# Kernel tuning notes

Measured on AMD Instinct MI355X. Metric: run time of the kernel, lower is better.

## Reference

```python
import jax, jax.numpy as jnp
import numpy as np

B, O, T, D, H, DOUT = 32, 4096, 16384, 128, 128, 128
EPS = 1e-3  # keras BatchNormalization default epsilon


def setup_inputs() -> dict:
    key = jax.random.key(0)
    ks = jax.random.split(key, 8)
    std = 0.05  # keras RandomNormal default stddev
    return {
        "obj_vecs": jax.random.normal(ks[0], (B, O, D), jnp.float32),
        "pred_vecs": jax.random.normal(ks[1], (B, T, D), jnp.float32),
        "edges": jax.random.randint(ks[2], (B, T, 2), 0, O, dtype=jnp.int32),
        # net1: [3D -> H] -> BN -> ReLU -> [H -> 2H+Dout] -> BN -> ReLU
        "W1": jax.random.normal(ks[3], (3 * D, H), jnp.float32) * std,
        "b1": jnp.zeros((H,), jnp.float32),
        "g1": jnp.ones((H,), jnp.float32),
        "be1": jnp.zeros((H,), jnp.float32),
        "W2": jax.random.normal(ks[4], (H, 2 * H + DOUT), jnp.float32) * std,
        "b2": jnp.zeros((2 * H + DOUT,), jnp.float32),
        "g2": jnp.ones((2 * H + DOUT,), jnp.float32),
        "be2": jnp.zeros((2 * H + DOUT,), jnp.float32),
        # net2: [H -> H] -> BN -> ReLU -> [H -> Dout] -> BN -> ReLU
        "W3": jax.random.normal(ks[5], (H, H), jnp.float32) * std,
        "b3": jnp.zeros((H,), jnp.float32),
        "g3": jnp.ones((H,), jnp.float32),
        "be3": jnp.zeros((H,), jnp.float32),
        "W4": jax.random.normal(ks[6], (H, DOUT), jnp.float32) * std,
        "b4": jnp.zeros((DOUT,), jnp.float32),
        "g4": jnp.ones((DOUT,), jnp.float32),
        "be4": jnp.zeros((DOUT,), jnp.float32),
    }


def _block(x, W, b, g, be):
    # Dense -> BatchNorm(inference: mean=0, var=1) -> ReLU
    h = x @ W + b
    h = h * (g / jnp.sqrt(1.0 + EPS)) + be
    return jax.nn.relu(h)


def reference(obj_vecs, pred_vecs, edges,
              W1, b1, g1, be1, W2, b2, g2, be2,
              W3, b3, g3, be3, W4, b4, g4, be4):
    s_idx = edges[..., 0]  # (B, T)
    o_idx = edges[..., 1]  # (B, T)

    # gather subject / object vectors: (B, T, D)
    cur_s = jnp.take_along_axis(obj_vecs, s_idx[..., None], axis=1)
    cur_o = jnp.take_along_axis(obj_vecs, o_idx[..., None], axis=1)
    cur_t = jnp.concatenate([cur_s, pred_vecs, cur_o], axis=2)  # (B, T, 3D)

    new_t = _block(_block(cur_t, W1, b1, g1, be1), W2, b2, g2, be2)  # (B, T, 2H+Dout)
    new_s = new_t[..., :H]
    new_p = new_t[..., H:H + DOUT]
    new_o = new_t[..., H + DOUT:]

    # NOTE: original TF code overwrites the s-scatter with the o-scatter,
    # so only object-side messages contribute. scatter_nd sums duplicates.
    bidx = jnp.arange(B)[:, None]  # (B, 1), broadcasts over T
    pooled = jnp.zeros((B, O, H), new_t.dtype).at[bidx, o_idx].add(new_o)
    counts = jnp.zeros((B, O), new_t.dtype).at[bidx, o_idx].add(1.0)
    pooled = pooled / jnp.clip(counts, 1.0, None)[..., None]  # avg pooling

    new_obj = _block(_block(pooled, W3, b3, g3, be3), W4, b4, g4, be4)  # (B, O, Dout)
    return new_obj, new_p
```

## Files before the change

### kernel.cpp

```cpp
#include <hip/hip_runtime.h>
#include <hip/hip_bf16.h>
#include <stdint.h>

#define Bn 32
#define On 4096
#define Tn 16384
#define Dn 128

typedef short short8 __attribute__((ext_vector_type(8)));
typedef float f32x4 __attribute__((ext_vector_type(4)));

__device__ inline short f2bf(float f) {
  union { float f; uint32_t u; } v; v.f = f;
  uint32_t u = v.u;
  uint32_t r = u + 0x7fffu + ((u >> 16) & 1u);
  return (short)(r >> 16);
}
__device__ inline float bf2f(unsigned short u) {
  union { uint32_t ui; float f; } cv; cv.ui = ((uint32_t)u) << 16; return cv.f;
}

#define LBAR() do { \
  asm volatile("s_waitcnt lgkmcnt(0)" ::: "memory"); \
  __builtin_amdgcn_sched_barrier(0); \
  __builtin_amdgcn_s_barrier(); \
} while (0)

__global__ void prep_weights(const float* __restrict__ W1, const float* __restrict__ W2,
                             const float* __restrict__ W3, const float* __restrict__ W4,
                             short* __restrict__ w1t, short* __restrict__ w2t,
                             short* __restrict__ w3t, short* __restrict__ w4t) {
  int i = blockIdx.x * 256 + threadIdx.x;
  if (i < 49152) {
    int n = i / 384, k = i % 384;
    w1t[i] = f2bf(W1[k * 128 + n]);
  } else if (i < 49152 + 32768) {
    int j = i - 49152;
    int n = j / 128, k = j % 128;
    w2t[j] = f2bf(W2[k * 384 + 128 + n]);
  } else if (i < 49152 + 32768 + 16384) {
    int j = i - 81920;
    int n = j / 128, k = j % 128;
    w3t[j] = f2bf(W3[k * 128 + n]);
  } else if (i < 114688) {
    int j = i - 98304;
    int n = j / 128, k = j % 128;
    w4t[j] = f2bf(W4[k * 128 + n]);
  }
}

__global__ __launch_bounds__(1024) void sort_kernel(
    const int* __restrict__ edges, int* __restrict__ hist_g,
    int* __restrict__ offs_g, unsigned short* __restrict__ eidx)
{
  __shared__ int h[4096];
  __shared__ int of[4096];
  __shared__ int sd[1024];
  int b = blockIdx.x, tid = threadIdx.x;
#pragma unroll
  for (int i = 0; i < 4; i++) h[tid + i * 1024] = 0;
  __syncthreads();
  int ov[16];
#pragma unroll
  for (int j = 0; j < 16; j++) {
    int t = j * 1024 + tid;
    ov[j] = edges[((size_t)(b * Tn + t)) * 2 + 1];
    atomicAdd(&h[ov[j]], 1);
  }
  __syncthreads();
  int base = tid * 4;
  int hh[4]; int s = 0;
#pragma unroll
  for (int j = 0; j < 4; j++) { hh[j] = h[base + j]; s += hh[j]; }
  sd[tid] = s;
  int tsum = s;
  for (int off = 1; off < 1024; off <<= 1) {
    __syncthreads();
    int t = (tid >= off) ? sd[tid - off] : 0;
    __syncthreads();
    sd[tid] += t;
  }
  __syncthreads();
  int excl = sd[tid] - tsum + b * Tn;
#pragma unroll
  for (int j = 0; j < 4; j++) {
    of[base + j] = excl;
    offs_g[b * On + base + j] = excl;
    hist_g[b * On + base + j] = hh[j];
    excl += hh[j];
  }
  __syncthreads();
#pragma unroll
  for (int i = 0; i < 4; i++) h[tid + i * 1024] = 0;
  __syncthreads();
#pragma unroll
  for (int j = 0; j < 16; j++) {
    int t = j * 1024 + tid;
    int pos = of[ov[j]] + atomicAdd(&h[ov[j]], 1);
    eidx[pos] = (unsigned short)t;
  }
}

__global__ __launch_bounds__(512, 2) void objproj(
    const float* __restrict__ obj, const short* __restrict__ w1t,
    unsigned short* __restrict__ objSO)
{
  __shared__ __align__(16) char lds[81920];
  const int WOF = 0, AOF = 65536;
  int tid = threadIdx.x;
  {
    int n = tid >> 2, q = tid & 3;
    int swz = (n & 7) << 4;
    const short* s1 = w1t + n * 384 + q * 32;
    const short* s2 = w1t + n * 384 + 256 + q * 32;
#pragma unroll
    for (int i = 0; i < 4; i++) {
      *(short8*)(lds + WOF + n * 256 + ((q * 64 + i * 16) ^ swz)) = *(const short8*)(s1 + i * 8);
      *(short8*)(lds + WOF + 32768 + n * 256 + ((q * 64 + i * 16) ^ swz)) = *(const short8*)(s2 + i * 8);
    }
  }
  int wave = tid >> 6, lane = tid & 63;
  int l15 = lane & 15, l4 = lane >> 4;
  int mg = wave >> 2, ng = wave & 3;
  int r = tid >> 3, seg = tid & 7;
  int rswz = (r & 7) << 4;

  for (int it = 0; it < 4; it++) {
    int row0 = (blockIdx.x * 4 + it) * 64;
    if (it) __syncthreads();
    {
      const float* src = obj + (size_t)(row0 + r) * Dn + seg * 16;
      float4 v0 = *(const float4*)(src);
      float4 v1 = *(const float4*)(src + 4);
      float4 v2 = *(const float4*)(src + 8);
      float4 v3 = *(const float4*)(src + 12);
      short8 p0, p1;
      p0[0]=f2bf(v0.x); p0[1]=f2bf(v0.y); p0[2]=f2bf(v0.z); p0[3]=f2bf(v0.w);
      p0[4]=f2bf(v1.x); p0[5]=f2bf(v1.y); p0[6]=f2bf(v1.z); p0[7]=f2bf(v1.w);
      p1[0]=f2bf(v2.x); p1[1]=f2bf(v2.y); p1[2]=f2bf(v2.z); p1[3]=f2bf(v2.w);
      p1[4]=f2bf(v3.x); p1[5]=f2bf(v3.y); p1[6]=f2bf(v3.z); p1[7]=f2bf(v3.w);
      *(short8*)(lds + AOF + r * 256 + ((seg * 32) ^ rswz)) = p0;
      *(short8*)(lds + AOF + r * 256 + ((seg * 32 + 16) ^ rswz)) = p1;
    }
    __syncthreads();
#pragma unroll
    for (int half = 0; half < 2; half++) {
      f32x4 acc[2][2] = {};
#pragma unroll
      for (int kk = 0; kk < 4; kk++) {
        short8 a[2], bb[2];
#pragma unroll
        for (int m = 0; m < 2; m++) {
          int row = mg * 32 + m * 16 + l15;
          a[m] = *(short8*)(lds + AOF + row * 256 + ((kk * 64 + 16 * l4) ^ ((row & 7) << 4)));
        }
#pragma unroll
        for (int n = 0; n < 2; n++) {
          int nr = ng * 32 + n * 16 + l15;
          bb[n] = *(short8*)(lds + WOF + half * 32768 + nr * 256 + ((kk * 64 + 16 * l4) ^ ((nr & 7) << 4)));
        }
#pragma unroll
        for (int m = 0; m < 2; m++)
#pragma unroll
          for (int n = 0; n < 2; n++)
            acc[m][n] = __builtin_amdgcn_mfma_f32_16x16x32_bf16(a[m], bb[n], acc[m][n], 0, 0, 0);
      }
#pragma unroll
      for (int n = 0; n < 2; n++) {
        int col = ng * 32 + n * 16 + l15;
#pragma unroll
        for (int m = 0; m < 2; m++)
#pragma unroll
          for (int rr = 0; rr < 4; rr++) {
            int row = mg * 32 + m * 16 + l4 * 4 + rr;
            objSO[(size_t)(row0 + row) * 256 + half * 128 + col] =
                (unsigned short)f2bf(acc[m][n][rr]);
          }
      }
    }
  }
}

#define ENT 32
__global__ __launch_bounds__(512, 2) void edge_mlp(
    const float* __restrict__ pred, const int* __restrict__ edges,
    const unsigned short* __restrict__ objSO,
    const short* __restrict__ w1t, const short* __restrict__ w2t,
    const float* __restrict__ b1, const float* __restrict__ g1, const float* __restrict__ be1,
    const float* __restrict__ b2, const float* __restrict__ g2, const float* __restrict__ be2,
    float* __restrict__ out_p, unsigned short* __restrict__ o_scr)
{
  __shared__ __align__(16) char lds[147456];
  const int W1P = 0;
  const int W2O = 32768;
  const int ABUF = 98304;
  const int HBUF = 114688;
  const int GOF = 131072;

  const float invs = 1.0f / sqrtf(1.001f);
  int tid = threadIdx.x;

  {
    int n = tid >> 2, q = tid & 3;
    int swz = (n & 7) << 4;
    const short* src = w1t + n * 384 + 128 + q * 32;
#pragma unroll
    for (int i = 0; i < 4; i++)
      *(short8*)(lds + W1P + n * 256 + ((q * 64 + i * 16) ^ swz)) = *(const short8*)(src + i * 8);
  }
  {
    int n = tid >> 1, q = tid & 1;
    int swz = (n & 7) << 4;
    const short* src = w2t + n * 128 + q * 64;
#pragma unroll
    for (int i = 0; i < 8; i++)
      *(short8*)(lds + W2O + n * 256 + ((q * 128 + i * 16) ^ swz)) = *(const short8*)(src + i * 8);
  }

  int r = tid >> 3, seg = tid & 7;
  int rswz = (r & 7) << 4;

  float4 pv0, pv1, pv2, pv3;
  short8 sv0, sv1, ov0, ov1;

  auto load_tile = [&](int gt) {
    int b_ = gt >> 8;
    int t = ((gt & 255) << 6) + r;
    const float* src = pred + ((size_t)(b_ * Tn + t)) * Dn + seg * 16;
    pv0 = *(const float4*)(src);
    pv1 = *(const float4*)(src + 4);
    pv2 = *(const float4*)(src + 8);
    pv3 = *(const float4*)(src + 12);
    int2 e = *(const int2*)&edges[((size_t)(b_ * Tn + t)) * 2];
    const unsigned short* srow = objSO + ((size_t)(b_ * On + e.x)) * 256 + seg * 16;
    const unsigned short* orow = objSO + ((size_t)(b_ * On + e.y)) * 256 + 128 + seg * 16;
    sv0 = *(const short8*)(srow);
    sv1 = *(const short8*)(srow + 8);
    ov0 = *(const short8*)(orow);
    ov1 = *(const short8*)(orow + 8);
  };

  auto store_stage = [&]() {
    short8 p0, p1;
    p0[0]=f2bf(pv0.x); p0[1]=f2bf(pv0.y); p0[2]=f2bf(pv0.z); p0[3]=f2bf(pv0.w);
    p0[4]=f2bf(pv1.x); p0[5]=f2bf(pv1.y); p0[6]=f2bf(pv1.z); p0[7]=f2bf(pv1.w);
    p1[0]=f2bf(pv2.x); p1[1]=f2bf(pv2.y); p1[2]=f2bf(pv2.z); p1[3]=f2bf(pv2.w);
    p1[4]=f2bf(pv3.x); p1[5]=f2bf(pv3.y); p1[6]=f2bf(pv3.z); p1[7]=f2bf(pv3.w);
    *(short8*)(lds + ABUF + r * 256 + ((seg * 32) ^ rswz)) = p0;
    *(short8*)(lds + ABUF + r * 256 + ((seg * 32 + 16) ^ rswz)) = p1;
    short8 g0, g1v;
#pragma unroll
    for (int j = 0; j < 8; j++) {
      g0[j]  = f2bf(bf2f((unsigned short)sv0[j]) + bf2f((unsigned short)ov0[j]));
      g1v[j] = f2bf(bf2f((unsigned short)sv1[j]) + bf2f((unsigned short)ov1[j]));
    }
    *(short8*)(lds + GOF + r * 256 + ((seg * 32) ^ rswz)) = g0;
    *(short8*)(lds + GOF + r * 256 + ((seg * 32 + 16) ^ rswz)) = g1v;
  };

  int tile0 = blockIdx.x * ENT;
  int wave = tid >> 6, lane = tid & 63;
  int l15 = lane & 15, l4 = lane >> 4;
  int mg = wave >> 2, ng = wave & 3;

  load_tile(tile0);
  store_stage();
  load_tile(tile0 + 1);
  LBAR();

  for (int k = 0; k < ENT; ++k) {
    int gt = tile0 + k;
    int b_ = gt >> 8, t0v = (gt & 255) << 6;

    f32x4 acc1[2][2] = {};
#pragma unroll
    for (int kk = 0; kk < 4; kk++) {
      short8 a[2], bb[2];
#pragma unroll
      for (int m = 0; m < 2; m++) {
        int row = mg * 32 + m * 16 + l15;
        a[m] = *(short8*)(lds + ABUF + row * 256 + ((kk * 64 + 16 * l4) ^ ((row & 7) << 4)));
      }
#pragma unroll
      for (int n = 0; n < 2; n++) {
        int nr = ng * 32 + n * 16 + l15;
        bb[n] = *(short8*)(lds + W1P + nr * 256 + ((kk * 64 + 16 * l4) ^ ((nr & 7) << 4)));
      }
#pragma unroll
      for (int m = 0; m < 2; m++)
#pragma unroll
        for (int n = 0; n < 2; n++)
          acc1[m][n] = __builtin_amdgcn_mfma_f32_16x16x32_bf16(a[m], bb[n], acc1[m][n], 0, 0, 0);
    }
#pragma unroll
    for (int n = 0; n < 2; n++) {
      int col = ng * 32 + n * 16 + l15;
      float gs = g1[col] * invs;
      float add = b1[col] * gs + be1[col];
#pragma unroll
      for (int m = 0; m < 2; m++)
#pragma unroll
        for (int rr = 0; rr < 4; rr++) {
          int row = mg * 32 + m * 16 + l4 * 4 + rr;
          float gv = bf2f(*(const unsigned short*)(lds + GOF + row * 256 + ((col * 2) ^ ((row & 7) << 4))));
          float v = fmaxf((acc1[m][n][rr] + gv) * gs + add, 0.0f);
          *(short*)(lds + HBUF + row * 256 + ((col * 2) ^ ((row & 7) << 4))) = f2bf(v);
        }
    }
    LBAR();

    if (k + 1 < ENT) store_stage();
    if (k + 2 < ENT) load_tile(tile0 + k + 2);

    f32x4 acc2[2][4] = {};
#pragma unroll
    for (int kk = 0; kk < 4; kk++) {
      short8 a[2], bb[4];
#pragma unroll
      for (int m = 0; m < 2; m++) {
        int row = mg * 32 + m * 16 + l15;
        a[m] = *(short8*)(lds + HBUF + row * 256 + ((kk * 64 + 16 * l4) ^ ((row & 7) << 4)));
      }
#pragma unroll
      for (int n = 0; n < 4; n++) {
        int nr = ng * 64 + n * 16 + l15;
        bb[n] = *(short8*)(lds + W2O + nr * 256 + ((kk * 64 + 16 * l4) ^ ((nr & 7) << 4)));
      }
#pragma unroll
      for (int m = 0; m < 2; m++)
#pragma unroll
        for (int n = 0; n < 4; n++)
          acc2[m][n] = __builtin_amdgcn_mfma_f32_16x16x32_bf16(a[m], bb[n], acc2[m][n], 0, 0, 0);
    }
#pragma unroll
    for (int n = 0; n < 4; n++) {
      int colp = ng * 64 + n * 16 + l15;
      int c2 = 128 + colp;
      float gs = g2[c2] * invs;
      float add = b2[c2] * gs + be2[c2];
#pragma unroll
      for (int m = 0; m < 2; m++)
#pragma unroll
        for (int rr = 0; rr < 4; rr++) {
          int row = mg * 32 + m * 16 + l4 * 4 + rr;
          float v = fmaxf(acc2[m][n][rr] * gs + add, 0.0f);
          if (colp < 128) {
            out_p[(size_t)(b_ * Tn + t0v + row) * 128 + colp] = v;
          } else {
            o_scr[(size_t)(b_ * Tn + t0v + row) * 128 + (colp - 128)] =
                (unsigned short)f2bf(v);
          }
        }
    }
    LBAR();
  }
}

__global__ __launch_bounds__(256) void obj_mlp(
    const unsigned short* __restrict__ o_scr, const int* __restrict__ hist,
    const int* __restrict__ offs, const unsigned short* __restrict__ eidx,
    float* __restrict__ out_obj,
    const short* __restrict__ w3t, const short* __restrict__ w4t,
    const float* __restrict__ b3, const float* __restrict__ g3, const float* __restrict__ be3,
    const float* __restrict__ b4, const float* __restrict__ g4, const float* __restrict__ be4)
{
  __shared__ short xs[64][136];
  __shared__ short hs[64][136];
  const float invs = 1.0f / sqrtf(1.001f);
  int row0 = blockIdx.x * 64;
  int tid = threadIdx.x;

  {
    int r = tid >> 2, seg = tid & 3;
    int rg = row0 + r;
    int bb_ = rg >> 12;
    int cnt = hist[rg], start = offs[rg];
    float sum[32];
#pragma unroll
    for (int j = 0; j < 32; j++) sum[j] = 0.f;
    for (int k = 0; k < cnt; k++) {
      int t = eidx[start + k];
      const unsigned short* src = o_scr + ((size_t)(bb_ * Tn + t)) * 128 + seg * 32;
#pragma unroll
      for (int i = 0; i < 4; i++) {
        short8 v = *(const short8*)(src + i * 8);
#pragma unroll
        for (int j = 0; j < 8; j++) sum[i * 8 + j] += bf2f((unsigned short)v[j]);
      }
    }
    float ic = 1.0f / fmaxf((float)cnt, 1.0f);
#pragma unroll
    for (int i = 0; i < 4; i++) {
      short8 pk;
#pragma unroll
      for (int j = 0; j < 8; j++) pk[j] = f2bf(sum[i * 8 + j] * ic);
      *(short8*)&xs[r][seg * 32 + i * 8] = pk;
    }
  }
  __syncthreads();

  int wave = tid >> 6, lane = tid & 63;
  int l15 = lane & 15, l4 = lane >> 4;
  int n0 = wave * 32;

  short8 w3r[2][4], w4r[2][4];
#pragma unroll
  for (int n = 0; n < 2; n++)
#pragma unroll
    for (int kk = 0; kk < 4; kk++) {
      w3r[n][kk] = *(const short8*)&w3t[(n0 + n * 16 + l15) * 128 + kk * 32 + 8 * l4];
      w4r[n][kk] = *(const short8*)&w4t[(n0 + n * 16 + l15) * 128 + kk * 32 + 8 * l4];
    }

  f32x4 acc[4][2] = {};
#pragma unroll
  for (int kk = 0; kk < 4; kk++) {
    int k0 = kk * 32;
    short8 a[4];
#pragma unroll
    for (int m = 0; m < 4; m++) a[m] = *(short8*)&xs[m * 16 + l15][k0 + 8 * l4];
#pragma unroll
    for (int m = 0; m < 4; m++)
#pragma unroll
      for (int n = 0; n < 2; n++)
        acc[m][n] = __builtin_amdgcn_mfma_f32_16x16x32_bf16(a[m], w3r[n][kk], acc[m][n], 0, 0, 0);
  }
#pragma unroll
  for (int n = 0; n < 2; n++) {
    int col = n0 + n * 16 + l15;
    float gs = g3[col] * invs;
    float add = b3[col] * gs + be3[col];
#pragma unroll
    for (int m = 0; m < 4; m++)
#pragma unroll
      for (int rr = 0; rr < 4; rr++) {
        float v = fmaxf(acc[m][n][rr] * gs + add, 0.0f);
        hs[m * 16 + l4 * 4 + rr][col] = f2bf(v);
      }
  }
  __syncthreads();

  f32x4 acc2[4][2] = {};
#pragma unroll
  for (int kk = 0; kk < 4; kk++) {
    int k0 = kk * 32;
    short8 a[4];
#pragma unroll
    for (int m = 0; m < 4; m++) a[m] = *(short8*)&hs[m * 16 + l15][k0 + 8 * l4];
#pragma unroll
    for (int m = 0; m < 4; m++)
#pragma unroll
      for (int n = 0; n < 2; n++)
        acc2[m][n] = __builtin_amdgcn_mfma_f32_16x16x32_bf16(a[m], w4r[n][kk], acc2[m][n], 0, 0, 0);
  }
#pragma unroll
  for (int n = 0; n < 2; n++) {
    int col = n0 + n * 16 + l15;
    float gs = g4[col] * invs;
    float add = b4[col] * gs + be4[col];
#pragma unroll
    for (int m = 0; m < 4; m++)
#pragma unroll
      for (int rr = 0; rr < 4; rr++) {
        int row = m * 16 + l4 * 4 + rr;
        float v = fmaxf(acc2[m][n][rr] * gs + add, 0.0f);
        out_obj[(size_t)(row0 + row) * 128 + col] = v;
      }
  }
}

extern "C" void kernel_launch(void* const* d_in, const int* in_sizes, int n_in,
                              void* d_out, int out_size, void* d_ws, size_t ws_size,
                              hipStream_t stream) {
  const float* obj  = (const float*)d_in[0];
  const float* pred = (const float*)d_in[1];
  const int*   edges= (const int*)d_in[2];
  const float* W1 = (const float*)d_in[3];
  const float* b1 = (const float*)d_in[4];
  const float* g1 = (const float*)d_in[5];
  const float* be1= (const float*)d_in[6];
  const float* W2 = (const float*)d_in[7];
  const float* b2 = (const float*)d_in[8];
  const float* g2 = (const float*)d_in[9];
  const float* be2= (const float*)d_in[10];
  const float* W3 = (const float*)d_in[11];
  const float* b3 = (const float*)d_in[12];
  const float* g3 = (const float*)d_in[13];
  const float* be3= (const float*)d_in[14];
  const float* W4 = (const float*)d_in[15];
  const float* b4 = (const float*)d_in[16];
  const float* g4 = (const float*)d_in[17];
  const float* be4= (const float*)d_in[18];

  float* out_obj = (float*)d_out;
  float* out_p   = (float*)d_out + (size_t)Bn * On * 128;
  unsigned short* objSO = (unsigned short*)d_out;

  char* ws = (char*)d_ws;
  short* w1t = (short*)(ws);
  short* w2t = (short*)(ws + 49152 * 2);
  short* w3t = (short*)(ws + (49152 + 32768) * 2);
  short* w4t = (short*)(ws + (49152 + 32768 + 16384) * 2);

  const size_t OFF_HIST = 262144;
  const size_t OFF_OFFS = OFF_HIST + 524288;
  const size_t OFF_EIDX = OFF_OFFS + 1048576;
  const size_t OFF_OSCR = 4194304;

  int* hist = (int*)(ws + OFF_HIST);
  int* offs = (int*)(ws + OFF_OFFS);
  unsigned short* eidx = (unsigned short*)(ws + OFF_EIDX);
  unsigned short* o_scr = (unsigned short*)(ws + OFF_OSCR);

  prep_weights<<<448, 256, 0, stream>>>(W1, W2, W3, W4, w1t, w2t, w3t, w4t);
  sort_kernel<<<Bn, 1024, 0, stream>>>(edges, hist, offs, eidx);
  objproj<<<512, 512, 0, stream>>>(obj, w1t, objSO);
  edge_mlp<<<256, 512, 0, stream>>>(pred, edges, objSO, w1t, w2t,
      b1, g1, be1, b2, g2, be2, out_p, o_scr);
  obj_mlp<<<(Bn * On) / 64, 256, 0, stream>>>(o_scr, hist, offs, eidx, out_obj,
      w3t, w4t, b3, g3, be3, b4, g4, be4);
}
```

Baseline: 324.4 us.

## Fold BN scale into weights and restructure edge MLP into per-wave register pipeline

Batch-norm scale and bias are folded into the bf16 weights and per-column add vectors during weight prep, which removes the scale and shift math from every epilogue. The edge MLP is rewritten so each wave independently owns 16-row strips. Predicate rows are loaded straight into registers as MFMA B-operands, and gathered subject and object rows are added in the epilogue. Only a per-wave LDS staging buffer is used for the hidden layer, so block-wide barriers and the shared A/gather staging buffers are gone. It adds s_setprio around the MFMA loops and prefetches the next strip's inputs. This trades LDS weight reads per wave, since there is no cross-wave reuse of A tiles, for fewer barriers and wider vector stores.

```diff
diff --git a/kernel.cpp b/kernel.cpp
--- a/kernel.cpp
+++ b/kernel.cpp
@@ -19,33 +19,53 @@
 __device__ inline float bf2f(unsigned short u) {
   union { uint32_t ui; float f; } cv; cv.ui = ((uint32_t)u) << 16; return cv.f;
 }
-
-#define LBAR() do { \
-  asm volatile("s_waitcnt lgkmcnt(0)" ::: "memory"); \
-  __builtin_amdgcn_sched_barrier(0); \
-  __builtin_amdgcn_s_barrier(); \
-} while (0)
+__device__ inline uint32_t pack2bf(float a, float b) {
+  return ((uint32_t)(uint16_t)f2bf(a)) | (((uint32_t)(uint16_t)f2bf(b)) << 16);
+}
+__device__ inline float bflo(uint32_t u) { union { uint32_t i; float f; } c; c.i = u << 16; return c.f; }
+__device__ inline float bfhi(uint32_t u) { union { uint32_t i; float f; } c; c.i = u & 0xffff0000u; return c.f; }
 
 __global__ void prep_weights(const float* __restrict__ W1, const float* __restrict__ W2,
                              const float* __restrict__ W3, const float* __restrict__ W4,
+                             const float* __restrict__ b1, const float* __restrict__ g1, const float* __restrict__ be1,
+                             const float* __restrict__ b2, const float* __restrict__ g2, const float* __restrict__ be2,
+                             const float* __restrict__ b3, const float* __restrict__ g3, const float* __restrict__ be3,
+                             const float* __restrict__ b4, const float* __restrict__ g4, const float* __restrict__ be4,
                              short* __restrict__ w1t, short* __restrict__ w2t,
-                             short* __restrict__ w3t, short* __restrict__ w4t) {
+                             short* __restrict__ w3t, short* __restrict__ w4t,
+                             float* __restrict__ add1g, float* __restrict__ add2g,
+                             float* __restrict__ add3g, float* __restrict__ add4g) {
+  const float invs = 1.0f / sqrtf(1.001f);
   int i = blockIdx.x * 256 + threadIdx.x;
   if (i < 49152) {
     int n = i / 384, k = i % 384;
-    w1t[i] = f2bf(W1[k * 128 + n]);
-  } else if (i < 49152 + 32768) {
+    w1t[i] = f2bf(W1[k * 128 + n] * g1[n] * invs);
+  } else if (i < 81920) {
     int j = i - 49152;
     int n = j / 128, k = j % 128;
-    w2t[j] = f2bf(W2[k * 384 + 128 + n]);
-  } else if (i < 49152 + 32768 + 16384) {
+    int c2 = 128 + n;
+    w2t[j] = f2bf(W2[k * 384 + c2] * g2[c2] * invs);
+  } else if (i < 98304) {
     int j = i - 81920;
     int n = j / 128, k = j % 128;
-    w3t[j] = f2bf(W3[k * 128 + n]);
+    w3t[j] = f2bf(W3[k * 128 + n] * g3[n] * invs);
   } else if (i < 114688) {
     int j = i - 98304;
     int n = j / 128, k = j % 128;
-    w4t[j] = f2bf(W4[k * 128 + n]);
+    w4t[j] = f2bf(W4[k * 128 + n] * g4[n] * invs);
+  } else if (i < 114816) {
+    int n = i - 114688;
+    add1g[n] = b1[n] * g1[n] * invs + be1[n];
+  } else if (i < 115072) {
+    int n = i - 114816;
+    int c2 = 128 + n;
+    add2g[n] = b2[c2] * g2[c2] * invs + be2[c2];
+  } else if (i < 115200) {
+    int n = i - 115072;
+    add3g[n] = b3[n] * g3[n] * invs + be3[n];
+  } else if (i < 115328) {
+    int n = i - 115200;
+    add4g[n] = b4[n] * g4[n] * invs + be4[n];
   }
 }
 
@@ -103,7 +123,7 @@
 
 __global__ __launch_bounds__(512, 2) void objproj(
     const float* __restrict__ obj, const short* __restrict__ w1t,
-    unsigned short* __restrict__ objSO)
+    const float* __restrict__ add1g, unsigned short* __restrict__ objSO)
 {
   __shared__ __align__(16) char lds[81920];
   const int WOF = 0, AOF = 65536;
@@ -168,38 +188,34 @@
 #pragma unroll
       for (int n = 0; n < 2; n++) {
         int col = ng * 32 + n * 16 + l15;
+        float addv = half ? 0.0f : add1g[col];
 #pragma unroll
         for (int m = 0; m < 2; m++)
 #pragma unroll
           for (int rr = 0; rr < 4; rr++) {
             int row = mg * 32 + m * 16 + l4 * 4 + rr;
             objSO[(size_t)(row0 + row) * 256 + half * 128 + col] =
-                (unsigned short)f2bf(acc[m][n][rr]);
+                (unsigned short)f2bf(acc[m][n][rr] + addv);
           }
       }
     }
   }
 }
 
-#define ENT 32
 __global__ __launch_bounds__(512, 2) void edge_mlp(
     const float* __restrict__ pred, const int* __restrict__ edges,
     const unsigned short* __restrict__ objSO,
     const short* __restrict__ w1t, const short* __restrict__ w2t,
-    const float* __restrict__ b1, const float* __restrict__ g1, const float* __restrict__ be1,
-    const float* __restrict__ b2, const float* __restrict__ g2, const float* __restrict__ be2,
+    const float* __restrict__ add2g,
     float* __restrict__ out_p, unsigned short* __restrict__ o_scr)
 {
-  __shared__ __align__(16) char lds[147456];
+  __shared__ __align__(16) char lds[132096];
   const int W1P = 0;
   const int W2O = 32768;
-  const int ABUF = 98304;
-  const int HBUF = 114688;
-  const int GOF = 131072;
-
-  const float invs = 1.0f / sqrtf(1.001f);
+  const int ADD2 = 98304;
+  const int H1B = 99328;
+
   int tid = threadIdx.x;
-
   {
     int n = tid >> 2, q = tid & 3;
     int swz = (n & 7) << 4;
@@ -216,143 +232,124 @@
     for (int i = 0; i < 8; i++)
       *(short8*)(lds + W2O + n * 256 + ((q * 128 + i * 16) ^ swz)) = *(const short8*)(src + i * 8);
   }
-
-  int r = tid >> 3, seg = tid & 7;
-  int rswz = (r & 7) << 4;
-
-  float4 pv0, pv1, pv2, pv3;
-  short8 sv0, sv1, ov0, ov1;
-
-  auto load_tile = [&](int gt) {
-    int b_ = gt >> 8;
-    int t = ((gt & 255) << 6) + r;
-    const float* src = pred + ((size_t)(b_ * Tn + t)) * Dn + seg * 16;
-    pv0 = *(const float4*)(src);
-    pv1 = *(const float4*)(src + 4);
-    pv2 = *(const float4*)(src + 8);
-    pv3 = *(const float4*)(src + 12);
-    int2 e = *(const int2*)&edges[((size_t)(b_ * Tn + t)) * 2];
-    const unsigned short* srow = objSO + ((size_t)(b_ * On + e.x)) * 256 + seg * 16;
-    const unsigned short* orow = objSO + ((size_t)(b_ * On + e.y)) * 256 + 128 + seg * 16;
-    sv0 = *(const short8*)(srow);
-    sv1 = *(const short8*)(srow + 8);
-    ov0 = *(const short8*)(orow);
-    ov1 = *(const short8*)(orow + 8);
-  };
-
-  auto store_stage = [&]() {
-    short8 p0, p1;
-    p0[0]=f2bf(pv0.x); p0[1]=f2bf(pv0.y); p0[2]=f2bf(pv0.z); p0[3]=f2bf(pv0.w);
-    p0[4]=f2bf(pv1.x); p0[5]=f2bf(pv1.y); p0[6]=f2bf(pv1.z); p0[7]=f2bf(pv1.w);
-    p1[0]=f2bf(pv2.x); p1[1]=f2bf(pv2.y); p1[2]=f2bf(pv2.z); p1[3]=f2bf(pv2.w);
-    p1[4]=f2bf(pv3.x); p1[5]=f2bf(pv3.y); p1[6]=f2bf(pv3.z); p1[7]=f2bf(pv3.w);
-    *(short8*)(lds + ABUF + r * 256 + ((seg * 32) ^ rswz)) = p0;
-    *(short8*)(lds + ABUF + r * 256 + ((seg * 32 + 16) ^ rswz)) = p1;
-    short8 g0, g1v;
-#pragma unroll
-    for (int j = 0; j < 8; j++) {
-      g0[j]  = f2bf(bf2f((unsigned short)sv0[j]) + bf2f((unsigned short)ov0[j]));
-      g1v[j] = f2bf(bf2f((unsigned short)sv1[j]) + bf2f((unsigned short)ov1[j]));
-    }
-    *(short8*)(lds + GOF + r * 256 + ((seg * 32) ^ rswz)) = g0;
-    *(short8*)(lds + GOF + r * 256 + ((seg * 32 + 16) ^ rswz)) = g1v;
-  };
-
-  int tile0 = blockIdx.x * ENT;
+  if (tid < 256) *(float*)(lds + ADD2 + tid * 4) = add2g[tid];
+  __syncthreads();
+
   int wave = tid >> 6, lane = tid & 63;
   int l15 = lane & 15, l4 = lane >> 4;
-  int mg = wave >> 2, ng = wave & 3;
-
-  load_tile(tile0);
-  store_stage();
-  load_tile(tile0 + 1);
-  LBAR();
-
-  for (int k = 0; k < ENT; ++k) {
-    int gt = tile0 + k;
-    int b_ = gt >> 8, t0v = (gt & 255) << 6;
-
-    f32x4 acc1[2][2] = {};
+  char* h1w = lds + H1B + wave * 4096;
+  int hswz = (l15 & 7) << 4;
+
+  size_t wrow0 = ((size_t)blockIdx.x * 8 + wave) * 256;
+  int b_ = (int)(wrow0 >> 14);
+  const char* soBase = (const char*)objSO + (size_t)b_ * On * 512;
+
+  float4 pp[8];
+  uint2 gsv[8], gov[8];
+  int2 e;
+
+  auto load_ep = [&](int j) {
+    size_t gr = wrow0 + (size_t)j * 16 + l15;
+    e = *(const int2*)&edges[gr * 2];
+    const float* pr = pred + gr * 128 + l4 * 8;
 #pragma unroll
     for (int kk = 0; kk < 4; kk++) {
-      short8 a[2], bb[2];
-#pragma unroll
-      for (int m = 0; m < 2; m++) {
-        int row = mg * 32 + m * 16 + l15;
-        a[m] = *(short8*)(lds + ABUF + row * 256 + ((kk * 64 + 16 * l4) ^ ((row & 7) << 4)));
-      }
-#pragma unroll
-      for (int n = 0; n < 2; n++) {
-        int nr = ng * 32 + n * 16 + l15;
-        bb[n] = *(short8*)(lds + W1P + nr * 256 + ((kk * 64 + 16 * l4) ^ ((nr & 7) << 4)));
-      }
-#pragma unroll
-      for (int m = 0; m < 2; m++)
-#pragma unroll
-        for (int n = 0; n < 2; n++)
-          acc1[m][n] = __builtin_amdgcn_mfma_f32_16x16x32_bf16(a[m], bb[n], acc1[m][n], 0, 0, 0);
-    }
-#pragma unroll
-    for (int n = 0; n < 2; n++) {
-      int col = ng * 32 + n * 16 + l15;
-      float gs = g1[col] * invs;
-      float add = b1[col] * gs + be1[col];
-#pragma unroll
-      for (int m = 0; m < 2; m++)
-#pragma unroll
-        for (int rr = 0; rr < 4; rr++) {
-          int row = mg * 32 + m * 16 + l4 * 4 + rr;
-          float gv = bf2f(*(const unsigned short*)(lds + GOF + row * 256 + ((col * 2) ^ ((row & 7) << 4))));
-          float v = fmaxf((acc1[m][n][rr] + gv) * gs + add, 0.0f);
-          *(short*)(lds + HBUF + row * 256 + ((col * 2) ^ ((row & 7) << 4))) = f2bf(v);
+      pp[2 * kk]     = *(const float4*)(pr + kk * 32);
+      pp[2 * kk + 1] = *(const float4*)(pr + kk * 32 + 4);
+    }
+  };
+  auto load_g = [&]() {
+    const char* bs = soBase + (size_t)e.x * 512 + l4 * 8;
+    const char* bo = soBase + (size_t)e.y * 512 + 256 + l4 * 8;
+#pragma unroll
+    for (int n = 0; n < 8; n++) {
+      gsv[n] = *(const uint2*)(bs + n * 32);
+      gov[n] = *(const uint2*)(bo + n * 32);
+    }
+  };
+
+  load_ep(0);
+  load_g();
+
+  for (int j = 0; j < 16; ++j) {
+    size_t gr = wrow0 + (size_t)j * 16 + l15;
+
+    short8 af[4];
+#pragma unroll
+    for (int kk = 0; kk < 4; kk++) {
+      float4 a0 = pp[2 * kk], a1 = pp[2 * kk + 1];
+      short8 a;
+      a[0]=f2bf(a0.x); a[1]=f2bf(a0.y); a[2]=f2bf(a0.z); a[3]=f2bf(a0.w);
+      a[4]=f2bf(a1.x); a[5]=f2bf(a1.y); a[6]=f2bf(a1.z); a[7]=f2bf(a1.w);
+      af[kk] = a;
+    }
+    if (j + 1 < 16) load_ep(j + 1);
+
+    f32x4 acc1[8] = {};
+    __builtin_amdgcn_s_setprio(1);
+#pragma unroll
+    for (int kk = 0; kk < 4; kk++) {
+#pragma unroll
+      for (int n = 0; n < 8; n++) {
+        short8 wf = *(short8*)(lds + W1P + (n * 16 + l15) * 256 + ((kk * 64 + 16 * l4) ^ hswz));
+        acc1[n] = __builtin_amdgcn_mfma_f32_16x16x32_bf16(wf, af[kk], acc1[n], 0, 0, 0);
+      }
+    }
+    __builtin_amdgcn_s_setprio(0);
+
+#pragma unroll
+    for (int n = 0; n < 8; n++) {
+      float v0 = fmaxf(acc1[n][0] + bflo(gsv[n].x) + bflo(gov[n].x), 0.0f);
+      float v1 = fmaxf(acc1[n][1] + bfhi(gsv[n].x) + bfhi(gov[n].x), 0.0f);
+      float v2 = fmaxf(acc1[n][2] + bflo(gsv[n].y) + bflo(gov[n].y), 0.0f);
+      float v3 = fmaxf(acc1[n][3] + bfhi(gsv[n].y) + bfhi(gov[n].y), 0.0f);
+      uint2 hd; hd.x = pack2bf(v0, v1); hd.y = pack2bf(v2, v3);
+      *(uint2*)(h1w + l15 * 256 + ((n * 32 + l4 * 8) ^ hswz)) = hd;
+    }
+    if (j + 1 < 16) load_g();
+
+    short8 af2[4];
+#pragma unroll
+    for (int kk = 0; kk < 4; kk++)
+      af2[kk] = *(short8*)(h1w + l15 * 256 + ((kk * 64 + 16 * l4) ^ hswz));
+
+#pragma unroll
+    for (int half = 0; half < 2; half++) {
+      f32x4 acc2[8] = {};
+      __builtin_amdgcn_s_setprio(1);
+#pragma unroll
+      for (int kk = 0; kk < 4; kk++) {
+#pragma unroll
+        for (int n = 0; n < 8; n++) {
+          short8 wf = *(short8*)(lds + W2O + (half * 128 + n * 16 + l15) * 256 + ((kk * 64 + 16 * l4) ^ hswz));
+          acc2[n] = __builtin_amdgcn_mfma_f32_16x16x32_bf16(wf, af2[kk], acc2[n], 0, 0, 0);
         }
-    }
-    LBAR();
-
-    if (k + 1 < ENT) store_stage();
-    if (k + 2 < ENT) load_tile(tile0 + k + 2);
-
-    f32x4 acc2[2][4] = {};
-#pragma unroll
-    for (int kk = 0; kk < 4; kk++) {
-      short8 a[2], bb[4];
-#pragma unroll
-      for (int m = 0; m < 2; m++) {
-        int row = mg * 32 + m * 16 + l15;
-        a[m] = *(short8*)(lds + HBUF + row * 256 + ((kk * 64 + 16 * l4) ^ ((row & 7) << 4)));
-      }
-#pragma unroll
-      for (int n = 0; n < 4; n++) {
-        int nr = ng * 64 + n * 16 + l15;
-        bb[n] = *(short8*)(lds + W2O + nr * 256 + ((kk * 64 + 16 * l4) ^ ((nr & 7) << 4)));
-      }
-#pragma unroll
-      for (int m = 0; m < 2; m++)
-#pragma unroll
-        for (int n = 0; n < 4; n++)
-          acc2[m][n] = __builtin_amdgcn_mfma_f32_16x16x32_bf16(a[m], bb[n], acc2[m][n], 0, 0, 0);
-    }
-#pragma unroll
-    for (int n = 0; n < 4; n++) {
-      int colp = ng * 64 + n * 16 + l15;
-      int c2 = 128 + colp;
-      float gs = g2[c2] * invs;
-      float add = b2[c2] * gs + be2[c2];
-#pragma unroll
-      for (int m = 0; m < 2; m++)
-#pragma unroll
-        for (int rr = 0; rr < 4; rr++) {
-          int row = mg * 32 + m * 16 + l4 * 4 + rr;
-          float v = fmaxf(acc2[m][n][rr] * gs + add, 0.0f);
-          if (colp < 128) {
-            out_p[(size_t)(b_ * Tn + t0v + row) * 128 + colp] = v;
-          } else {
-            o_scr[(size_t)(b_ * Tn + t0v + row) * 128 + (colp - 128)] =
-                (unsigned short)f2bf(v);
-          }
+      }
+      __builtin_amdgcn_s_setprio(0);
+      if (half == 0) {
+#pragma unroll
+        for (int n = 0; n < 8; n++) {
+          float4 ad = *(float4*)(lds + ADD2 + (n * 16 + l4 * 4) * 4);
+          float4 ov;
+          ov.x = fmaxf(acc2[n][0] + ad.x, 0.0f);
+          ov.y = fmaxf(acc2[n][1] + ad.y, 0.0f);
+          ov.z = fmaxf(acc2[n][2] + ad.z, 0.0f);
+          ov.w = fmaxf(acc2[n][3] + ad.w, 0.0f);
+          *(float4*)(out_p + gr * 128 + n * 16 + l4 * 4) = ov;
         }
-    }
-    LBAR();
+      } else {
+#pragma unroll
+        for (int n = 0; n < 8; n++) {
+          float4 ad = *(float4*)(lds + ADD2 + 512 + (n * 16 + l4 * 4) * 4);
+          float v0 = fmaxf(acc2[n][0] + ad.x, 0.0f);
+          float v1 = fmaxf(acc2[n][1] + ad.y, 0.0f);
+          float v2 = fmaxf(acc2[n][2] + ad.z, 0.0f);
+          float v3 = fmaxf(acc2[n][3] + ad.w, 0.0f);
+          uint2 od; od.x = pack2bf(v0, v1); od.y = pack2bf(v2, v3);
+          *(uint2*)((char*)o_scr + gr * 256 + (n * 16 + l4 * 4) * 2) = od;
+        }
+      }
+    }
   }
 }
 
@@ -361,12 +358,10 @@
     const int* __restrict__ offs, const unsigned short* __restrict__ eidx,
     float* __restrict__ out_obj,
     const short* __restrict__ w3t, const short* __restrict__ w4t,
-    const float* __restrict__ b3, const float* __restrict__ g3, const float* __restrict__ be3,
-    const float* __restrict__ b4, const float* __restrict__ g4, const float* __restrict__ be4)
+    const float* __restrict__ add3g, const float* __restrict__ add4g)
 {
   __shared__ short xs[64][136];
   __shared__ short hs[64][136];
-  const float invs = 1.0f / sqrtf(1.001f);
   int row0 = blockIdx.x * 64;
   int tid = threadIdx.x;
 
@@ -428,13 +423,12 @@
 #pragma unroll
   for (int n = 0; n < 2; n++) {
     int col = n0 + n * 16 + l15;
-    float gs = g3[col] * invs;
-    float add = b3[col] * gs + be3[col];
+    float ad = add3g[col];
 #pragma unroll
     for (int m = 0; m < 4; m++)
 #pragma unroll
       for (int rr = 0; rr < 4; rr++) {
-        float v = fmaxf(acc[m][n][rr] * gs + add, 0.0f);
+        float v = fmaxf(acc[m][n][rr] + ad, 0.0f);
         hs[m * 16 + l4 * 4 + rr][col] = f2bf(v);
       }
   }
@@ -456,14 +450,13 @@
 #pragma unroll
   for (int n = 0; n < 2; n++) {
     int col = n0 + n * 16 + l15;
-    float gs = g4[col] * invs;
-    float add = b4[col] * gs + be4[col];
+    float ad = add4g[col];
 #pragma unroll
     for (int m = 0; m < 4; m++)
 #pragma unroll
       for (int rr = 0; rr < 4; rr++) {
         int row = m * 16 + l4 * 4 + rr;
-        float v = fmaxf(acc2[m][n][rr] * gs + add, 0.0f);
+        float v = fmaxf(acc2[m][n][rr] + ad, 0.0f);
         out_obj[(size_t)(row0 + row) * 128 + col] = v;
       }
   }
@@ -501,6 +494,10 @@
   short* w2t = (short*)(ws + 49152 * 2);
   short* w3t = (short*)(ws + (49152 + 32768) * 2);
   short* w4t = (short*)(ws + (49152 + 32768 + 16384) * 2);
+  float* add1g = (float*)(ws + 229376);
+  float* add2g = (float*)(ws + 229888);
+  float* add3g = (float*)(ws + 230912);
+  float* add4g = (float*)(ws + 231424);
 
   const size_t OFF_HIST = 262144;
   const size_t OFF_OFFS = OFF_HIST + 524288;
@@ -512,11 +509,13 @@
   unsigned short* eidx = (unsigned short*)(ws + OFF_EIDX);
   unsigned short* o_scr = (unsigned short*)(ws + OFF_OSCR);
 
-  prep_weights<<<448, 256, 0, stream>>>(W1, W2, W3, W4, w1t, w2t, w3t, w4t);
+  prep_weights<<<451, 256, 0, stream>>>(W1, W2, W3, W4,
+      b1, g1, be1, b2, g2, be2, b3, g3, be3, b4, g4, be4,
+      w1t, w2t, w3t, w4t, add1g, add2g, add3g, add4g);
   sort_kernel<<<Bn, 1024, 0, stream>>>(edges, hist, offs, eidx);
-  objproj<<<512, 512, 0, stream>>>(obj, w1t, objSO);
-  edge_mlp<<<256, 512, 0, stream>>>(pred, edges, objSO, w1t, w2t,
-      b1, g1, be1, b2, g2, be2, out_p, o_scr);
+  objproj<<<512, 512, 0, stream>>>(obj, w1t, add1g, objSO);
+  edge_mlp<<<256, 512, 0, stream>>>(pred, edges, objSO, w1t, w2t, add2g,
+      out_p, o_scr);
   obj_mlp<<<(Bn * On) / 64, 256, 0, stream>>>(o_scr, hist, offs, eidx, out_obj,
-      w3t, w4t, b3, g3, be3, b4, g4, be4);
-}
+      w3t, w4t, add3g, add4g);
+}
```

Result: no change. 327.3 us (+0.9%).
